# Performance work log

Measured on AMD Instinct MI355X. Metric: run time of the kernel, lower is better.

## Reference

```python
import jax, jax.numpy as jnp
import numpy as np

VOCAB, DIM, HEADS, LAYERS = 32000, 1024, 16, 2
B, S = 2, 1024
HD = DIM // HEADS


def rmsnorm(x, g, eps=1e-6):
    return x * jax.lax.rsqrt(jnp.mean(x * x, axis=-1, keepdims=True) + eps) * g


def setup_inputs() -> dict:
    key = jax.random.key(0)
    ks = jax.random.split(key, 20)
    s = 0.02
    d = {
        "text_ids": jax.random.randint(ks[0], (B, S), 0, VOCAB),
        "embed": jax.random.normal(ks[1], (VOCAB, DIM), jnp.float32) * s,
        "g1": jnp.ones((LAYERS, DIM), jnp.float32),
        "wq": jax.random.normal(ks[2], (LAYERS, DIM, DIM), jnp.float32) * s,
        "bq": jnp.zeros((LAYERS, DIM), jnp.float32),
        "wk": jax.random.normal(ks[3], (LAYERS, DIM, DIM), jnp.float32) * s,
        "bk": jnp.zeros((LAYERS, DIM), jnp.float32),
        "wv": jax.random.normal(ks[4], (LAYERS, DIM, DIM), jnp.float32) * s,
        "bv": jnp.zeros((LAYERS, DIM), jnp.float32),
        "wo": jax.random.normal(ks[5], (LAYERS, DIM, DIM), jnp.float32) * s,
        "bo": jnp.zeros((LAYERS, DIM), jnp.float32),
        "g2": jnp.ones((LAYERS, DIM), jnp.float32),
        "w1": jax.random.normal(ks[6], (LAYERS, DIM, 4 * DIM), jnp.float32) * s,
        "b1": jnp.zeros((LAYERS, 4 * DIM), jnp.float32),
        "w2": jax.random.normal(ks[7], (LAYERS, 4 * DIM, DIM), jnp.float32) * s,
        "b2": jnp.zeros((LAYERS, DIM), jnp.float32),
        "gf": jnp.ones((DIM,), jnp.float32),
        "head_w": jax.random.normal(ks[8], (DIM, VOCAB), jnp.float32) * s,
        "head_b": jnp.zeros((VOCAB,), jnp.float32),
    }
    return d


def reference(text_ids, embed, g1, wq, bq, wk, bk, wv, bv, wo, bo,
              g2, w1, b1, w2, b2, gf, head_w, head_b):
    b, s = text_ids.shape
    x = embed[text_ids]                                   # [B,S,D]
    causal = jnp.tril(jnp.ones((s, s), dtype=bool))        # [S,S]
    scale = 1.0 / jnp.sqrt(jnp.asarray(HD, x.dtype))
    for l in range(LAYERS):
        # attention sublayer: x = x + attn(norm1(x))
        h = rmsnorm(x, g1[l])
        q = (h @ wq[l] + bq[l]).reshape(b, s, HEADS, HD)
        k = (h @ wk[l] + bk[l]).reshape(b, s, HEADS, HD)
        v = (h @ wv[l] + bv[l]).reshape(b, s, HEADS, HD)
        scores = jnp.einsum("bqhd,bkhd->bhqk", q, k) * scale
        scores = jnp.where(causal, scores, jnp.asarray(-1e30, scores.dtype))
        a = jax.nn.softmax(scores, axis=-1)
        o = jnp.einsum("bhqk,bkhd->bqhd", a, v).reshape(b, s, DIM)
        x = x + (o @ wo[l] + bo[l])
        # FFN sublayer: x = x + ffn(norm2(x)), SiLU MLP (MoE unused in source forward)
        h2 = rmsnorm(x, g2[l])
        x = x + (jax.nn.silu(h2 @ w1[l] + b1[l]) @ w2[l] + b2[l])
    x = rmsnorm(x, gf)
    return x.astype(jnp.float32) @ head_w + head_b         # [B,S,VOCAB]
```

## Files before the change

### kernel.cpp

```cpp
#include <hip/hip_runtime.h>

#define LAYERS 2
#define DIM 1024
#define HEADS 16
#define HD 64
#define BATCH 2
#define SEQ 1024
#define ROWS (BATCH * SEQ)
#define FFN (4 * DIM)
#define VOCAB 32000
#define QKVN (3 * DIM)

typedef unsigned short u16;
typedef short vshort8 __attribute__((ext_vector_type(8)));
typedef float f32x4 __attribute__((ext_vector_type(4)));

#define VMCNT(n) asm volatile("s_waitcnt vmcnt(" #n ")" ::: "memory")

__device__ __forceinline__ u16 f2bf(float f) {
  union { float f; unsigned u; } x{f};
  unsigned r = (x.u + 0x7fffu + ((x.u >> 16) & 1u)) >> 16;
  return (u16)r;
}

__device__ __forceinline__ void gll16(const void* g, u16* l) {
  __builtin_amdgcn_global_load_lds(
      (const __attribute__((address_space(1))) void*)g,
      (__attribute__((address_space(3))) void*)l, 16, 0, 0);
}

__device__ __forceinline__ int xcd_swizzle(int orig, int nwg) {
  int q = nwg >> 3, r = nwg & 7;
  int xcd = orig & 7;
  int base = (xcd < r) ? xcd * (q + 1) : r * (q + 1) + (xcd - r) * q;
  return base + (orig >> 3);
}

__device__ __forceinline__ void trans64(const float* __restrict__ src,
                                        u16* __restrict__ dst, int C, int R,
                                        int r0, int c0, int tid,
                                        u16 (*tl)[72]) {
  int lr = tid >> 4, lc4 = (tid & 15) * 4;
#pragma unroll
  for (int i = 0; i < 4; i++) {
    int row = lr + i * 16;
    float4 v = *(const float4*)&src[(size_t)(r0 + row) * C + c0 + lc4];
    ushort4 o{f2bf(v.x), f2bf(v.y), f2bf(v.z), f2bf(v.w)};
    *(ushort4*)&tl[row][lc4] = o;
  }
  __syncthreads();
#pragma unroll
  for (int i = 0; i < 2; i++) {
    int idx = tid + i * 256;
    int ci = idx >> 3, ri0 = (idx & 7) * 8;
    vshort8 o;
#pragma unroll
    for (int j = 0; j < 8; j++) o[j] = (short)tl[ri0 + j][ci];
    *(vshort8*)&dst[(size_t)(c0 + ci) * R + r0 + ri0] = o;
  }
}

__global__ __launch_bounds__(256) void prologue_kernel(
    const float* __restrict__ wq, const float* __restrict__ wk,
    const float* __restrict__ wv, const float* __restrict__ wo,
    const float* __restrict__ w1, const float* __restrict__ w2,
    const float* __restrict__ head_w, const float* __restrict__ bq,
    const float* __restrict__ bk, const float* __restrict__ bv,
    const int* __restrict__ ids, const float* __restrict__ emb,
    const float* __restrict__ g1, u16* __restrict__ wqkvT,
    u16* __restrict__ woT, u16* __restrict__ w1T, u16* __restrict__ w2T,
    u16* __restrict__ headT, float* __restrict__ bqkv, float* __restrict__ x,
    u16* __restrict__ h) {
  __shared__ u16 tl[64][72];
  __shared__ float part[4];
  int bid = blockIdx.x, tid = threadIdx.x;
  if (bid >= 6144 && bid < 6168) {
    int t = (bid - 6144) * 256 + tid;
    int l = t / QKVN, c = t % QKVN;
    float v;
    if (c < DIM) v = bq[l * DIM + c];
    else if (c < 2 * DIM) v = bk[l * DIM + c - DIM];
    else v = bv[l * DIM + c - 2 * DIM];
    bqkv[(size_t)l * QKVN + c] = v;
    return;
  }
  if (bid >= 6168 && bid < 8216) {
    int row = bid - 6168;
    int id = ids[row];
    float4 v = ((const float4*)(emb + (size_t)id * DIM))[tid];
    ((float4*)(x + (size_t)row * DIM))[tid] = v;
    float ss = v.x * v.x + v.y * v.y + v.z * v.z + v.w * v.w;
    for (int off = 32; off > 0; off >>= 1) ss += __shfl_down(ss, off);
    if ((tid & 63) == 0) part[tid >> 6] = ss;
    __syncthreads();
    float tot = part[0] + part[1] + part[2] + part[3];
    float r = rsqrtf(tot / (float)DIM + 1e-6f);
    float4 gv = ((const float4*)g1)[tid];
    ushort4 o;
    o.x = f2bf(v.x * r * gv.x);
    o.y = f2bf(v.y * r * gv.y);
    o.z = f2bf(v.z * r * gv.z);
    o.w = f2bf(v.w * r * gv.w);
    *(ushort4*)(h + (size_t)row * DIM + tid * 4) = o;
    return;
  }
  const float* src;
  u16* dst;
  int R, C, r0, c0;
  if (bid < 2048) {
    int job = bid >> 8, tile = bid & 255;
    int l = job >> 2, wsel = job & 3;
    src = (wsel == 0 ? wq : wsel == 1 ? wk : wsel == 2 ? wv : wo) +
          (size_t)l * DIM * DIM;
    dst = (wsel < 3)
              ? wqkvT + (size_t)l * QKVN * DIM + (size_t)wsel * DIM * DIM
              : woT + (size_t)l * DIM * DIM;
    R = DIM; C = DIM;
    c0 = (tile & 15) * 64; r0 = (tile >> 4) * 64;
  } else if (bid < 4096) {
    int idx = bid - 2048;
    int l = idx >> 10, t = idx & 1023;
    src = w1 + (size_t)l * DIM * FFN;
    dst = w1T + (size_t)l * DIM * FFN;
    R = DIM; C = FFN;
    c0 = (t & 63) * 64; r0 = (t >> 6) * 64;
  } else if (bid < 6144) {
    int idx = bid - 4096;
    int l = idx >> 10, t = idx & 1023;
    src = w2 + (size_t)l * FFN * DIM;
    dst = w2T + (size_t)l * FFN * DIM;
    R = FFN; C = DIM;
    c0 = (t & 15) * 64; r0 = (t >> 4) * 64;
  } else {
    int t = bid - 8216;
    src = head_w; dst = headT;
    R = DIM; C = VOCAB;
    c0 = (t % 500) * 64; r0 = (t / 500) * 64;
  }
  trans64(src, dst, C, R, r0, c0, tid, tl);
}

template <int NP>
__global__ __launch_bounds__(256) void addnorm_kernel(
    float* __restrict__ x, const float* __restrict__ P,
    const float* __restrict__ bias, const float* __restrict__ g,
    u16* __restrict__ h) {
  int row = blockIdx.x;
  int t = threadIdx.x;
  float4 v = ((const float4*)(x + (size_t)row * DIM))[t];
  float4 c = ((const float4*)bias)[t];
  v.x += c.x; v.y += c.y; v.z += c.z; v.w += c.w;
#pragma unroll
  for (int p = 0; p < NP; p++) {
    float4 a = ((const float4*)(P + (size_t)p * ROWS * DIM + (size_t)row * DIM))[t];
    v.x += a.x; v.y += a.y; v.z += a.z; v.w += a.w;
  }
  ((float4*)(x + (size_t)row * DIM))[t] = v;
  float ss = v.x * v.x + v.y * v.y + v.z * v.z + v.w * v.w;
  for (int off = 32; off > 0; off >>= 1) ss += __shfl_down(ss, off);
  __shared__ float part[4];
  if ((t & 63) == 0) part[t >> 6] = ss;
  __syncthreads();
  float tot = part[0] + part[1] + part[2] + part[3];
  float r = rsqrtf(tot / (float)DIM + 1e-6f);
  float4 gv = ((const float4*)g)[t];
  ushort4 o;
  o.x = f2bf(v.x * r * gv.x);
  o.y = f2bf(v.y * r * gv.y);
  o.z = f2bf(v.z * r * gv.z);
  o.w = f2bf(v.w * r * gv.w);
  *(ushort4*)(h + (size_t)row * DIM + t * 4) = o;
}

template <int NMT, int OUTF32, int SILU, int VT>
__global__ __launch_bounds__(512, 2) void gemm256x128p_kernel(
    const u16* __restrict__ A, const u16* __restrict__ Wt,
    const float* __restrict__ bias, void* __restrict__ outv,
    u16* __restrict__ vt2, int M, int N, int K) {
  __shared__ u16 As[3][256 * 64];
  __shared__ u16 Bs[3][128 * 64];
  int nm = M >> 8, nn = N >> 7;
  int nwg = (NMT == 1) ? nm * nn : nn;
  int wg = xcd_swizzle(blockIdx.x, nwg);
  int mi0, ni;
  if (NMT == 1) { mi0 = wg % nm; ni = wg / nm; }
  else          { mi0 = 0; ni = wg; }
  int n0 = ni << 7;
  int tid = threadIdx.x, w = tid >> 6, lane = tid & 63;
  int wr = w >> 1, wc = w & 1;
  int r16 = lane & 15, g4 = lane >> 4;
  int srow8 = lane >> 3, sslot = lane & 7;
  const int NG = NMT * 16;

  f32x4 acc[4][4] = {};

  auto stage = [&](int g) {
    int buf = g % 3;
    int kt = g & 15;
    int mb = (mi0 + (g >> 4)) << 8;
#pragma unroll
    for (int j = 0; j < 4; j++) {
      int chunk = j * 8 + w;
      int row = chunk * 8 + srow8;
      int slot = sslot ^ (row & 7);
      gll16(A + (size_t)(mb + row) * K + kt * 64 + slot * 8,
            &As[buf][chunk * 512 + lane * 8]);
    }
#pragma unroll
    for (int j = 0; j < 2; j++) {
      int chunk = j * 8 + w;
      int row = chunk * 8 + srow8;
      int slot = sslot ^ (row & 7);
      gll16(Wt + (size_t)(n0 + row) * K + kt * 64 + slot * 8,
            &Bs[buf][chunk * 512 + lane * 8]);
    }
  };
  auto readA = [&](int buf, int mf, int kk) -> vshort8 {
    int row = wr * 64 + mf * 16 + r16;
    int slot = (kk * 4 + g4) ^ (row & 7);
    return *(const vshort8*)&As[buf][row * 64 + slot * 8];
  };
  auto readB = [&](int buf, int nf, int kk) -> vshort8 {
    int row = wc * 64 + nf * 16 + r16;
    int slot = (kk * 4 + g4) ^ (row & 7);
    return *(const vshort8*)&Bs[buf][row * 64 + slot * 8];
  };

  stage(0);
  stage(1);
  VMCNT(6);
  __builtin_amdgcn_s_barrier();

  vshort8 af[4][2], bf0[2][2], bf1[2][2];

  for (int mt = 0; mt < NMT; mt++) {
    for (int kt = 0; kt < 16; kt++) {
      int g = mt * 16 + kt;
      int buf = g % 3;
#pragma unroll
      for (int m = 0; m < 4; m++)
#pragma unroll
        for (int kk = 0; kk < 2; kk++) af[m][kk] = readA(buf, m, kk);
#pragma unroll
      for (int n = 0; n < 2; n++)
#pragma unroll
        for (int kk = 0; kk < 2; kk++) bf0[n][kk] = readB(buf, n, kk);
      bool staged = (g + 2 < NG);
      if (staged) stage(g + 2);
      __builtin_amdgcn_s_barrier();
      __builtin_amdgcn_s_setprio(1);
#pragma unroll
      for (int m = 0; m < 4; m++)
#pragma unroll
        for (int n = 0; n < 2; n++)
#pragma unroll
          for (int kk = 0; kk < 2; kk++)
            acc[m][n] = __builtin_amdgcn_mfma_f32_16x16x32_bf16(
                af[m][kk], bf0[n][kk], acc[m][n], 0, 0, 0);
      __builtin_amdgcn_s_setprio(0);
      __builtin_amdgcn_s_barrier();
#pragma unroll
      for (int n = 0; n < 2; n++)
#pragma unroll
        for (int kk = 0; kk < 2; kk++) bf1[n][kk] = readB(buf, 2 + n, kk);
      __builtin_amdgcn_s_barrier();
      __builtin_amdgcn_s_setprio(1);
#pragma unroll
      for (int m = 0; m < 4; m++)
#pragma unroll
        for (int n = 0; n < 2; n++)
#pragma unroll
          for (int kk = 0; kk < 2; kk++)
            acc[m][n + 2] = __builtin_amdgcn_mfma_f32_16x16x32_bf16(
                af[m][kk], bf1[n][kk], acc[m][n + 2], 0, 0, 0);
      __builtin_amdgcn_s_setprio(0);
      if (staged) { VMCNT(6); } else { VMCNT(0); }
      __builtin_amdgcn_s_barrier();
    }
    int m0e = (mi0 + mt) << 8;
#pragma unroll
    for (int m = 0; m < 4; m++) {
      int rowb = m0e + wr * 64 + m * 16 + g4 * 4;
#pragma unroll
      for (int n = 0; n < 4; n++) {
        int col = n0 + wc * 64 + n * 16 + r16;
        float b = bias[col];
        if (OUTF32) {
#pragma unroll
          for (int j = 0; j < 4; j++)
            ((float*)outv)[(size_t)(rowb + j) * N + col] = acc[m][n][j] + b;
        } else {
          u16 ov[4];
#pragma unroll
          for (int j = 0; j < 4; j++) {
            float v = acc[m][n][j] + b;
            if (SILU) v = v / (1.f + __expf(-v));
            ov[j] = f2bf(v);
          }
          if (VT && col >= 2 * DIM) {
            int dv = col - 2 * DIM;
            int hh = dv >> 6, dd = dv & 63;
            int bb = rowb >> 10, s = rowb & 1023;
            ushort4 o4{ov[0], ov[1], ov[2], ov[3]};
            *(ushort4*)&vt2[((((size_t)(bb * 16 + hh) * (SEQ / 8) + (s >> 3)) *
                                  64 + dd) * 8) + (s & 7)] = o4;
          } else {
#pragma unroll
            for (int j = 0; j < 4; j++)
              ((u16*)outv)[(size_t)(rowb + j) * N + col] = ov[j];
          }
        }
        if (NMT > 1) acc[m][n] = f32x4{0.f, 0.f, 0.f, 0.f};
      }
    }
  }
}

template <int NS>
__global__ __launch_bounds__(256, 2) void gemm128sk_kernel(
    const u16* __restrict__ A, const u16* __restrict__ Wt,
    float* __restrict__ P, int M, int N, int K) {
  __shared__ u16 As[2][128 * 64];
  __shared__ u16 Bs[2][128 * 64];
  int nm = M >> 7, nn = N >> 7, nwg = nm * nn;
  int wg = xcd_swizzle(blockIdx.x, nwg * NS);
  int ks = wg / nwg;
  wg -= ks * nwg;
  int ni = wg % nn, mi = wg / nn;
  int m0 = mi << 7, n0 = ni << 7;
  int kb = ks * (K / NS);
  int NTt = (K / NS) >> 6;
  int tid = threadIdx.x, wave = tid >> 6, lane = tid & 63;
  int wr = wave >> 1, wc = wave & 1;
  int r16 = lane & 15, g4 = lane >> 4;
  int lrow = lane >> 3, lslot = lane & 7;

  f32x4 acc[4][4] = {};

  auto stage = [&](int buf, int kt) {
#pragma unroll
    for (int i = 0; i < 4; i++) {
      int s = wave * 4 + i;
      int row = s * 8 + lrow;
      int slot = lslot ^ (row & 7);
      gll16(A + (size_t)(m0 + row) * K + kb + kt * 64 + slot * 8,
            &As[buf][s * 512 + lane * 8]);
    }
#pragma unroll
    for (int i = 0; i < 4; i++) {
      int s = wave * 4 + i;
      int row = s * 8 + lrow;
      int slot = lslot ^ (row & 7);
      gll16(Wt + (size_t)(n0 + row) * K + kb + kt * 64 + slot * 8,
            &Bs[buf][s * 512 + lane * 8]);
    }
  };

  stage(0, 0);
  VMCNT(0);
  __builtin_amdgcn_s_barrier();

  for (int t = 0; t < NTt; t++) {
    int cur = t & 1;
    if (t + 1 < NTt) stage(cur ^ 1, t + 1);
#pragma unroll
    for (int kk = 0; kk < 2; kk++) {
      vshort8 af[4], bf[4];
#pragma unroll
      for (int m = 0; m < 4; m++) {
        int r = wr * 64 + m * 16 + r16;
        int slot = (kk * 4 + g4) ^ (r & 7);
        af[m] = *(const vshort8*)&As[cur][r * 64 + slot * 8];
      }
#pragma unroll
      for (int n = 0; n < 4; n++) {
        int c = wc * 64 + n * 16 + r16;
        int slot = (kk * 4 + g4) ^ (c & 7);
        bf[n] = *(const vshort8*)&Bs[cur][c * 64 + slot * 8];
      }
#pragma unroll
      for (int m = 0; m < 4; m++)
#pragma unroll
        for (int n = 0; n < 4; n++)
          acc[m][n] = __builtin_amdgcn_mfma_f32_16x16x32_bf16(af[m], bf[n],
                                                              acc[m][n], 0, 0, 0);
    }
    VMCNT(0);
    __builtin_amdgcn_s_barrier();
  }

  float* Pk = P + (size_t)ks * M * N;
#pragma unroll
  for (int m = 0; m < 4; m++) {
    int rowb = m0 + wr * 64 + m * 16 + g4 * 4;
#pragma unroll
    for (int n = 0; n < 4; n++) {
      int col = n0 + wc * 64 + n * 16 + r16;
#pragma unroll
      for (int j = 0; j < 4; j++)
        Pk[(size_t)(rowb + j) * N + col] = acc[m][n][j];
    }
  }
}

__global__ __launch_bounds__(512, 2) void gemm256p_kernel(
    const u16* __restrict__ A, const u16* __restrict__ Wt,
    const float* __restrict__ bias, float* __restrict__ out,
    int M, int N, int K) {
  __shared__ u16 As[2][256 * 64];
  __shared__ u16 Bs[2][256 * 64];
  int nn = N >> 8;
  int wg = xcd_swizzle(blockIdx.x, nn * 2);
  int ni = wg >> 1, mhalf = wg & 1;
  int n0 = ni << 8;
  int tid = threadIdx.x, w = tid >> 6, lane = tid & 63;
  int wr = w >> 2, wc = w & 3;
  int r16 = lane & 15, g4 = lane >> 4;
  int srow8 = lane >> 3, sslot = lane & 7;
  const int NTK = 16;
  const int NGT = 64;

  f32x4 acc[8][4] = {};

  auto stageA = [&](int buf, int mb, int kt, int hb, int j) {
    int chunk = j * 8 + w;
    int row = hb * 128 + chunk * 8 + srow8;
    int slot = sslot ^ (row & 7);
    gll16(A + (size_t)(mb + row) * K + kt * 64 + slot * 8,
          &As[buf][hb * 8192 + chunk * 512 + lane * 8]);
  };
  auto stageB = [&](int buf, int kt, int hb, int j) {
    int chunk = j * 8 + w;
    int row = hb * 128 + chunk * 8 + srow8;
    int slot = sslot ^ (row & 7);
    gll16(Wt + (size_t)(n0 + row) * K + kt * 64 + slot * 8,
          &Bs[buf][hb * 8192 + chunk * 512 + lane * 8]);
  };
  auto readA = [&](int buf, int mf, int kk) -> vshort8 {
    int row = mf * 32 + wr * 16 + r16;
    int slot = (kk * 4 + g4) ^ (row & 7);
    return *(const vshort8*)&As[buf][row * 64 + slot * 8];
  };
  auto readB = [&](int buf, int nf, int kk) -> vshort8 {
    int row = nf * 64 + wc * 16 + r16;
    int slot = (kk * 4 + g4) ^ (row & 7);
    return *(const vshort8*)&Bs[buf][row * 64 + slot * 8];
  };

  int mb0 = (mhalf * 4) << 8;
  stageA(0, mb0, 0, 0, 0); stageA(0, mb0, 0, 0, 1);
  stageB(0, 0, 0, 0);      stageB(0, 0, 0, 1);
  stageB(0, 0, 1, 0);      stageB(0, 0, 1, 1);
  stageA(0, mb0, 0, 1, 0); stageA(0, mb0, 0, 1, 1);
  VMCNT(4);
  __builtin_amdgcn_s_barrier();

  vshort8 af[4][2], bf0[2][2], bf1[2][2];

  for (int ti = 0; ti < 4; ti++) {
    int m0 = (mhalf * 4 + ti) << 8;
    for (int tt = 0; tt < NTK; tt++) {
      int gt = ti * NTK + tt;
      int cur = gt & 1, nxt = cur ^ 1;
      int gt1 = gt + 1;
      bool hn = gt1 < NGT;
      int kt1 = gt1 & (NTK - 1);
      int mb1 = (mhalf * 4 + (gt1 >> 4)) << 8;
#pragma unroll
      for (int m = 0; m < 4; m++)
#pragma unroll
        for (int kk = 0; kk < 2; kk++) af[m][kk] = readA(cur, m, kk);
#pragma unroll
      for (int n = 0; n < 2; n++)
#pragma unroll
        for (int kk = 0; kk < 2; kk++) bf0[n][kk] = readB(cur, n, kk);
      if (hn) {
        stageA(nxt, mb1, kt1, 0, 0); stageA(nxt, mb1, kt1, 0, 1);
        stageB(nxt, kt1, 0, 0);      stageB(nxt, kt1, 0, 1);
      }
      __builtin_amdgcn_s_barrier();
      __builtin_amdgcn_s_setprio(1);
#pragma unroll
      for (int m = 0; m < 4; m++)
#pragma unroll
        for (int n = 0; n < 2; n++)
#pragma unroll
          for (int kk = 0; kk < 2; kk++)
            acc[m][n] = __builtin_amdgcn_mfma_f32_16x16x32_bf16(
                af[m][kk], bf0[n][kk], acc[m][n], 0, 0, 0);
      __builtin_amdgcn_s_setprio(0);
      VMCNT(4);
      __builtin_amdgcn_s_barrier();
#pragma unroll
      for (int n = 0; n < 2; n++)
#pragma unroll
        for (int kk = 0; kk < 2; kk++) bf1[n][kk] = readB(cur, 2 + n, kk);
      __builtin_amdgcn_s_barrier();
      __builtin_amdgcn_s_setprio(1);
#pragma unroll
      for (int m = 0; m < 4; m++)
#pragma unroll
        for (int n = 0; n < 2; n++)
#pragma unroll
          for (int kk = 0; kk < 2; kk++)
            acc[m][n + 2] = __builtin_amdgcn_mfma_f32_16x16x32_bf16(
                af[m][kk], bf1[n][kk], acc[m][n + 2], 0, 0, 0);
      __builtin_amdgcn_s_setprio(0);
      __builtin_amdgcn_s_barrier();
#pragma unroll
      for (int m = 0; m < 4; m++)
#pragma unroll
        for (int kk = 0; kk < 2; kk++) af[m][kk] = readA(cur, 4 + m, kk);
      if (hn) {
        stageB(nxt, kt1, 1, 0);      stageB(nxt, kt1, 1, 1);
        stageA(nxt, mb1, kt1, 1, 0); stageA(nxt, mb1, kt1, 1, 1);
      }
      __builtin_amdgcn_s_barrier();
      __builtin_amdgcn_s_setprio(1);
#pragma unroll
      for (int m = 0; m < 4; m++)
#pragma unroll
        for (int n = 0; n < 2; n++)
#pragma unroll
          for (int kk = 0; kk < 2; kk++)
            acc[m + 4][n + 2] = __builtin_amdgcn_mfma_f32_16x16x32_bf16(
                af[m][kk], bf1[n][kk], acc[m + 4][n + 2], 0, 0, 0);
#pragma unroll
      for (int m = 0; m < 4; m++)
#pragma unroll
        for (int n = 0; n < 2; n++)
#pragma unroll
          for (int kk = 0; kk < 2; kk++)
            acc[m + 4][n] = __builtin_amdgcn_mfma_f32_16x16x32_bf16(
                af[m][kk], bf0[n][kk], acc[m + 4][n], 0, 0, 0);
      __builtin_amdgcn_s_setprio(0);
      VMCNT(4);
      __builtin_amdgcn_s_barrier();
    }
#pragma unroll
    for (int mf = 0; mf < 8; mf++) {
      int rowb = m0 + mf * 32 + wr * 16 + g4 * 4;
#pragma unroll
      for (int nf = 0; nf < 4; nf++) {
        int col = n0 + nf * 64 + wc * 16 + r16;
        float b = bias[col];
#pragma unroll
        for (int j = 0; j < 4; j++)
          out[(size_t)(rowb + j) * N + col] = acc[mf][nf][j] + b;
      }
    }
#pragma unroll
    for (int mf = 0; mf < 8; mf++)
#pragma unroll
      for (int nf = 0; nf < 4; nf++) acc[mf][nf] = f32x4{0.f, 0.f, 0.f, 0.f};
  }
}

__global__ __launch_bounds__(256) void attn_kernel(const u16* __restrict__ qkv,
                                                   const u16* __restrict__ vt2,
                                                   u16* __restrict__ o) {
  __shared__ u16 Ks[2][32 * 64];
  __shared__ u16 pl[4][16 * 40];
  int qblk = blockIdx.x, bh = blockIdx.y;
  int b = bh >> 4, h = bh & 15;
  int tid = threadIdx.x, w = tid >> 6, lane = tid & 63;
  int r16 = lane & 15, g4 = lane >> 4;
  int q0 = qblk * 64 + w * 16;

  const u16* qrow = qkv + ((size_t)(b * SEQ) + q0 + r16) * QKVN + h * HD;
  vshort8 aq0 = *(const vshort8*)(qrow + g4 * 8);
  vshort8 aq1 = *(const vshort8*)(qrow + 32 + g4 * 8);

  float mrun[4], lrun[4];
  f32x4 accO[4];
#pragma unroll
  for (int j = 0; j < 4; j++) { mrun[j] = -1e30f; lrun[j] = 0.f; }
#pragma unroll
  for (int d = 0; d < 4; d++) accO[d] = f32x4{0.f, 0.f, 0.f, 0.f};

  int nkvT = qblk * 2 + 2;
  auto stageK = [&](int buf, int kt) {
    int row = tid >> 3;
    int slot = (tid & 7) ^ (row & 7);
    gll16(qkv + ((size_t)(b * SEQ) + kt * 32 + row) * QKVN + DIM + h * HD + slot * 8,
          &Ks[buf][w * 512 + lane * 8]);
  };
  stageK(0, 0);
  __syncthreads();
  int buf = 0;
  for (int kt = 0; kt < nkvT; kt++) {
    int kv0 = kt * 32;
    if (kt + 1 < nkvT) stageK(buf ^ 1, kt + 1);
    if (kv0 <= q0 + 15) {
      int row0 = r16, row1 = 16 + r16;
      vshort8 bk00 = *(const vshort8*)&Ks[buf][row0 * 64 + ((0 + g4) ^ (row0 & 7)) * 8];
      vshort8 bk01 = *(const vshort8*)&Ks[buf][row0 * 64 + ((4 + g4) ^ (row0 & 7)) * 8];
      vshort8 bk10 = *(const vshort8*)&Ks[buf][row1 * 64 + ((0 + g4) ^ (row1 & 7)) * 8];
      vshort8 bk11 = *(const vshort8*)&Ks[buf][row1 * 64 + ((4 + g4) ^ (row1 & 7)) * 8];
      f32x4 s0 = {}, s1 = {};
      s0 = __builtin_amdgcn_mfma_f32_16x16x32_bf16(aq0, bk00, s0, 0, 0, 0);
      s0 = __builtin_amdgcn_mfma_f32_16x16x32_bf16(aq1, bk01, s0, 0, 0, 0);
      s1 = __builtin_amdgcn_mfma_f32_16x16x32_bf16(aq0, bk10, s1, 0, 0, 0);
      s1 = __builtin_amdgcn_mfma_f32_16x16x32_bf16(aq1, bk11, s1, 0, 0, 0);

#pragma unroll
      for (int j = 0; j < 4; j++) {
        int qg = q0 + g4 * 4 + j;
        float x0 = s0[j] * 0.125f;
        float x1 = s1[j] * 0.125f;
        if (kv0 + r16 > qg) x0 = -1e30f;
        if (kv0 + 16 + r16 > qg) x1 = -1e30f;
        float mx = fmaxf(x0, x1);
#pragma unroll
        for (int mm = 1; mm < 16; mm <<= 1) mx = fmaxf(mx, __shfl_xor(mx, mm));
        float mnew = fmaxf(mrun[j], mx);
        float alpha = __expf(mrun[j] - mnew);
        float p0 = __expf(x0 - mnew);
        float p1 = __expf(x1 - mnew);
        float rs = p0 + p1;
#pragma unroll
        for (int mm = 1; mm < 16; mm <<= 1) rs += __shfl_xor(rs, mm);
        lrun[j] = lrun[j] * alpha + rs;
        mrun[j] = mnew;
#pragma unroll
        for (int d = 0; d < 4; d++) accO[d][j] *= alpha;
        pl[w][(g4 * 4 + j) * 40 + r16] = f2bf(p0);
        pl[w][(g4 * 4 + j) * 40 + 16 + r16] = f2bf(p1);
      }
      asm volatile("s_waitcnt lgkmcnt(0)" ::: "memory");
      vshort8 ap = *(const vshort8*)&pl[w][r16 * 40 + g4 * 8];
      const u16* vbase = vt2 + (((size_t)bh * (SEQ / 8) + (kv0 >> 3) + g4) * 64) * 8;
#pragma unroll
      for (int d = 0; d < 4; d++) {
        vshort8 bv = *(const vshort8*)(vbase + (size_t)(d * 16 + r16) * 8);
        accO[d] = __builtin_amdgcn_mfma_f32_16x16x32_bf16(ap, bv, accO[d], 0, 0, 0);
      }
    }
    __syncthreads();
    buf ^= 1;
  }

#pragma unroll
  for (int j = 0; j < 4; j++) {
    float inv = 1.f / lrun[j];
    int row = q0 + g4 * 4 + j;
#pragma unroll
    for (int d = 0; d < 4; d++)
      o[((size_t)(b * SEQ) + row) * DIM + h * HD + d * 16 + r16] =
          f2bf(accO[d][j] * inv);
  }
}

extern "C" void kernel_launch(void* const* d_in, const int* in_sizes, int n_in,
                              void* d_out, int out_size, void* d_ws,
                              size_t ws_size, hipStream_t stream) {
  const int* ids = (const int*)d_in[0];
  const float* emb = (const float*)d_in[1];
  const float* g1 = (const float*)d_in[2];
  const float* wq = (const float*)d_in[3];
  const float* bq = (const float*)d_in[4];
  const float* wk = (const float*)d_in[5];
  const float* bk = (const float*)d_in[6];
  const float* wv = (const float*)d_in[7];
  const float* bv = (const float*)d_in[8];
  const float* wo = (const float*)d_in[9];
  const float* bo = (const float*)d_in[10];
  const float* g2 = (const float*)d_in[11];
  const float* w1 = (const float*)d_in[12];
  const float* b1 = (const float*)d_in[13];
  const float* w2 = (const float*)d_in[14];
  const float* b2 = (const float*)d_in[15];
  const float* gf = (const float*)d_in[16];
  const float* head_w = (const float*)d_in[17];
  const float* head_b = (const float*)d_in[18];
  float* out = (float*)d_out;

  char* ws = (char*)d_ws;
  size_t off = 0;
  auto alloc = [&](size_t bytes) -> char* {
    char* p = ws + off;
    off += (bytes + 255) & ~(size_t)255;
    return p;
  };
  u16* wqkvT = (u16*)alloc((size_t)LAYERS * QKVN * DIM * 2);
  u16* woT = (u16*)alloc((size_t)LAYERS * DIM * DIM * 2);
  u16* w1T = (u16*)alloc((size_t)LAYERS * DIM * FFN * 2);
  u16* w2T = (u16*)alloc((size_t)LAYERS * DIM * FFN * 2);
  u16* headT = (u16*)alloc((size_t)VOCAB * DIM * 2);
  float* bqkv = (float*)alloc((size_t)LAYERS * QKVN * 4);
  float* x = (float*)alloc((size_t)ROWS * DIM * 4);
  u16* h = (u16*)alloc((size_t)ROWS * DIM * 2);
  u16* qkvb = (u16*)alloc((size_t)ROWS * QKVN * 2);
  u16* vtb = (u16*)alloc((size_t)ROWS * DIM * 2);
  u16* ob = (u16*)alloc((size_t)ROWS * DIM * 2);
  u16* tb = (u16*)alloc((size_t)ROWS * FFN * 2);
  float* P = (float*)alloc((size_t)4 * ROWS * DIM * 4);
  if (off > ws_size) return;

  prologue_kernel<<<16216, 256, 0, stream>>>(
      wq, wk, wv, wo, w1, w2, head_w, bq, bk, bv, ids, emb, g1, wqkvT, woT,
      w1T, w2T, headT, bqkv, x, h);

  for (int l = 0; l < LAYERS; l++) {
    gemm256x128p_kernel<1, 0, 0, 1>
        <<<(ROWS / 256) * (QKVN / 128), 512, 0, stream>>>(
            h, wqkvT + (size_t)l * QKVN * DIM, bqkv + (size_t)l * QKVN,
            qkvb, vtb, ROWS, QKVN, DIM);
    attn_kernel<<<dim3(SEQ / 64, BATCH * HEADS), 256, 0, stream>>>(qkvb, vtb, ob);
    gemm128sk_kernel<4>
        <<<4 * (ROWS / 128) * (DIM / 128), 256, 0, stream>>>(
            ob, woT + (size_t)l * DIM * DIM, P, ROWS, DIM, DIM);
    addnorm_kernel<4><<<ROWS, 256, 0, stream>>>(
        x, P, bo + (size_t)l * DIM, g2 + (size_t)l * DIM, h);
    gemm256x128p_kernel<1, 0, 1, 0>
        <<<(ROWS / 256) * (FFN / 128), 512, 0, stream>>>(
            h, w1T + (size_t)l * DIM * FFN, b1 + (size_t)l * FFN, tb, nullptr,
            ROWS, FFN, DIM);
    gemm128sk_kernel<4>
        <<<4 * (ROWS / 128) * (DIM / 128), 256, 0, stream>>>(
            tb, w2T + (size_t)l * DIM * FFN, P, ROWS, DIM, FFN);
    addnorm_kernel<4><<<ROWS, 256, 0, stream>>>(
        x, P, b2 + (size_t)l * DIM,
        (l == LAYERS - 1) ? gf : (g1 + (size_t)(l + 1) * DIM), h);
  }
  gemm256p_kernel<<<(VOCAB / 256) * 2, 512, 0, stream>>>(
      h, headT, head_b, out, ROWS, VOCAB, DIM);
}
```

Baseline: 558.6 us.

## Rewrite LM-head GEMM with triple-buffered K=32 stages and a single MFMA phase

Replaces the double-buffered K=64 LM-head GEMM, which split each step into several MFMA phases with interleaved loads and barriers, with a triple-buffered pipeline over K=32 tiles that prefetches two stages ahead. Each iteration now does one block of LDS reads, one issue of global-to-LDS loads and one MFMA burst, with a single barrier per step, and uses a new XOR swizzle for the narrower tiles. Launch bounds drop from two blocks per CU to one. The intent is to hide memory latency with fewer barriers, at the cost of occupancy and of twice as many k-steps, each carrying a barrier.

```diff
diff --git a/kernel.cpp b/kernel.cpp
--- a/kernel.cpp
+++ b/kernel.cpp
@@ -403,12 +403,12 @@
   }
 }
 
-__global__ __launch_bounds__(512, 2) void gemm256p_kernel(
+__global__ __launch_bounds__(512, 1) void gemm256h_kernel(
     const u16* __restrict__ A, const u16* __restrict__ Wt,
     const float* __restrict__ bias, float* __restrict__ out,
     int M, int N, int K) {
-  __shared__ u16 As[2][256 * 64];
-  __shared__ u16 Bs[2][256 * 64];
+  __shared__ u16 As[3][256 * 32];
+  __shared__ u16 Bs[3][256 * 32];
   int nn = N >> 8;
   int wg = xcd_swizzle(blockIdx.x, nn * 2);
   int ni = wg >> 1, mhalf = wg & 1;
@@ -416,143 +416,81 @@
   int tid = threadIdx.x, w = tid >> 6, lane = tid & 63;
   int wr = w >> 2, wc = w & 3;
   int r16 = lane & 15, g4 = lane >> 4;
-  int srow8 = lane >> 3, sslot = lane & 7;
-  const int NTK = 16;
-  const int NGT = 64;
+  const int NG = 128;
 
   f32x4 acc[8][4] = {};
 
-  auto stageA = [&](int buf, int mb, int kt, int hb, int j) {
-    int chunk = j * 8 + w;
-    int row = hb * 128 + chunk * 8 + srow8;
-    int slot = sslot ^ (row & 7);
-    gll16(A + (size_t)(mb + row) * K + kt * 64 + slot * 8,
-          &As[buf][hb * 8192 + chunk * 512 + lane * 8]);
+  int srow = w * 16 + (lane >> 2);
+  int schunk = lane & 3;
+
+  auto stage = [&](int g) {
+    int buf = g % 3;
+    int kt = g & 31;
+    int mb = (mhalf * 4 + (g >> 5)) << 8;
+#pragma unroll
+    for (int u = 0; u < 2; u++) {
+      int row = u * 128 + srow;
+      int klog = (schunk ^ ((row >> 1) & 3)) * 8;
+      gll16(A + (size_t)(mb + row) * K + kt * 32 + klog,
+            &As[buf][u * 4096 + w * 512 + lane * 8]);
+    }
+#pragma unroll
+    for (int u = 0; u < 2; u++) {
+      int row = u * 128 + srow;
+      int klog = (schunk ^ ((row >> 1) & 3)) * 8;
+      gll16(Wt + (size_t)(n0 + row) * K + kt * 32 + klog,
+            &Bs[buf][u * 4096 + w * 512 + lane * 8]);
+    }
   };
-  auto stageB = [&](int buf, int kt, int hb, int j) {
-    int chunk = j * 8 + w;
-    int row = hb * 128 + chunk * 8 + srow8;
-    int slot = sslot ^ (row & 7);
-    gll16(Wt + (size_t)(n0 + row) * K + kt * 64 + slot * 8,
-          &Bs[buf][hb * 8192 + chunk * 512 + lane * 8]);
-  };
-  auto readA = [&](int buf, int mf, int kk) -> vshort8 {
-    int row = mf * 32 + wr * 16 + r16;
-    int slot = (kk * 4 + g4) ^ (row & 7);
-    return *(const vshort8*)&As[buf][row * 64 + slot * 8];
-  };
-  auto readB = [&](int buf, int nf, int kk) -> vshort8 {
-    int row = nf * 64 + wc * 16 + r16;
-    int slot = (kk * 4 + g4) ^ (row & 7);
-    return *(const vshort8*)&Bs[buf][row * 64 + slot * 8];
-  };
-
-  int mb0 = (mhalf * 4) << 8;
-  stageA(0, mb0, 0, 0, 0); stageA(0, mb0, 0, 0, 1);
-  stageB(0, 0, 0, 0);      stageB(0, 0, 0, 1);
-  stageB(0, 0, 1, 0);      stageB(0, 0, 1, 1);
-  stageA(0, mb0, 0, 1, 0); stageA(0, mb0, 0, 1, 1);
+
+  stage(0);
+  stage(1);
   VMCNT(4);
   __builtin_amdgcn_s_barrier();
 
-  vshort8 af[4][2], bf0[2][2], bf1[2][2];
-
-  for (int ti = 0; ti < 4; ti++) {
-    int m0 = (mhalf * 4 + ti) << 8;
-    for (int tt = 0; tt < NTK; tt++) {
-      int gt = ti * NTK + tt;
-      int cur = gt & 1, nxt = cur ^ 1;
-      int gt1 = gt + 1;
-      bool hn = gt1 < NGT;
-      int kt1 = gt1 & (NTK - 1);
-      int mb1 = (mhalf * 4 + (gt1 >> 4)) << 8;
-#pragma unroll
-      for (int m = 0; m < 4; m++)
-#pragma unroll
-        for (int kk = 0; kk < 2; kk++) af[m][kk] = readA(cur, m, kk);
-#pragma unroll
-      for (int n = 0; n < 2; n++)
-#pragma unroll
-        for (int kk = 0; kk < 2; kk++) bf0[n][kk] = readB(cur, n, kk);
-      if (hn) {
-        stageA(nxt, mb1, kt1, 0, 0); stageA(nxt, mb1, kt1, 0, 1);
-        stageB(nxt, kt1, 0, 0);      stageB(nxt, kt1, 0, 1);
+  for (int g = 0; g < NG; g++) {
+    int buf = g % 3;
+    vshort8 af[8], bf[4];
+#pragma unroll
+    for (int m = 0; m < 8; m++) {
+      int row = m * 32 + wr * 16 + r16;
+      int s = g4 ^ ((row >> 1) & 3);
+      af[m] = *(const vshort8*)&As[buf][row * 32 + s * 8];
+    }
+#pragma unroll
+    for (int n = 0; n < 4; n++) {
+      int row = n * 64 + wc * 16 + r16;
+      int s = g4 ^ ((row >> 1) & 3);
+      bf[n] = *(const vshort8*)&Bs[buf][row * 32 + s * 8];
+    }
+    bool staged = (g + 2 < NG);
+    if (staged) stage(g + 2);
+    __builtin_amdgcn_s_setprio(1);
+#pragma unroll
+    for (int m = 0; m < 8; m++)
+#pragma unroll
+      for (int n = 0; n < 4; n++)
+        acc[m][n] = __builtin_amdgcn_mfma_f32_16x16x32_bf16(af[m], bf[n],
+                                                            acc[m][n], 0, 0, 0);
+    __builtin_amdgcn_s_setprio(0);
+    if (staged) { VMCNT(4); } else { VMCNT(0); }
+    __builtin_amdgcn_s_barrier();
+    if ((g & 31) == 31) {
+      int m0 = (mhalf * 4 + (g >> 5)) << 8;
+#pragma unroll
+      for (int mf = 0; mf < 8; mf++) {
+        int rowb = m0 + mf * 32 + wr * 16 + g4 * 4;
+#pragma unroll
+        for (int nf = 0; nf < 4; nf++) {
+          int col = n0 + nf * 64 + wc * 16 + r16;
+          float b = bias[col];
+#pragma unroll
+          for (int j = 0; j < 4; j++)
+            out[(size_t)(rowb + j) * N + col] = acc[mf][nf][j] + b;
+          acc[mf][nf] = f32x4{0.f, 0.f, 0.f, 0.f};
+        }
       }
-      __builtin_amdgcn_s_barrier();
-      __builtin_amdgcn_s_setprio(1);
-#pragma unroll
-      for (int m = 0; m < 4; m++)
-#pragma unroll
-        for (int n = 0; n < 2; n++)
-#pragma unroll
-          for (int kk = 0; kk < 2; kk++)
-            acc[m][n] = __builtin_amdgcn_mfma_f32_16x16x32_bf16(
-                af[m][kk], bf0[n][kk], acc[m][n], 0, 0, 0);
-      __builtin_amdgcn_s_setprio(0);
-      VMCNT(4);
-      __builtin_amdgcn_s_barrier();
-#pragma unroll
-      for (int n = 0; n < 2; n++)
-#pragma unroll
-        for (int kk = 0; kk < 2; kk++) bf1[n][kk] = readB(cur, 2 + n, kk);
-      __builtin_amdgcn_s_barrier();
-      __builtin_amdgcn_s_setprio(1);
-#pragma unroll
-      for (int m = 0; m < 4; m++)
-#pragma unroll
-        for (int n = 0; n < 2; n++)
-#pragma unroll
-          for (int kk = 0; kk < 2; kk++)
-            acc[m][n + 2] = __builtin_amdgcn_mfma_f32_16x16x32_bf16(
-                af[m][kk], bf1[n][kk], acc[m][n + 2], 0, 0, 0);
-      __builtin_amdgcn_s_setprio(0);
-      __builtin_amdgcn_s_barrier();
-#pragma unroll
-      for (int m = 0; m < 4; m++)
-#pragma unroll
-        for (int kk = 0; kk < 2; kk++) af[m][kk] = readA(cur, 4 + m, kk);
-      if (hn) {
-        stageB(nxt, kt1, 1, 0);      stageB(nxt, kt1, 1, 1);
-        stageA(nxt, mb1, kt1, 1, 0); stageA(nxt, mb1, kt1, 1, 1);
-      }
-      __builtin_amdgcn_s_barrier();
-      __builtin_amdgcn_s_setprio(1);
-#pragma unroll
-      for (int m = 0; m < 4; m++)
-#pragma unroll
-        for (int n = 0; n < 2; n++)
-#pragma unroll
-          for (int kk = 0; kk < 2; kk++)
-            acc[m + 4][n + 2] = __builtin_amdgcn_mfma_f32_16x16x32_bf16(
-                af[m][kk], bf1[n][kk], acc[m + 4][n + 2], 0, 0, 0);
-#pragma unroll
-      for (int m = 0; m < 4; m++)
-#pragma unroll
-        for (int n = 0; n < 2; n++)
-#pragma unroll
-          for (int kk = 0; kk < 2; kk++)
-            acc[m + 4][n] = __builtin_amdgcn_mfma_f32_16x16x32_bf16(
-                af[m][kk], bf0[n][kk], acc[m + 4][n], 0, 0, 0);
-      __builtin_amdgcn_s_setprio(0);
-      VMCNT(4);
-      __builtin_amdgcn_s_barrier();
-    }
-#pragma unroll
-    for (int mf = 0; mf < 8; mf++) {
-      int rowb = m0 + mf * 32 + wr * 16 + g4 * 4;
-#pragma unroll
-      for (int nf = 0; nf < 4; nf++) {
-        int col = n0 + nf * 64 + wc * 16 + r16;
-        float b = bias[col];
-#pragma unroll
-        for (int j = 0; j < 4; j++)
-          out[(size_t)(rowb + j) * N + col] = acc[mf][nf][j] + b;
-      }
-    }
-#pragma unroll
-    for (int mf = 0; mf < 8; mf++)
-#pragma unroll
-      for (int nf = 0; nf < 4; nf++) acc[mf][nf] = f32x4{0.f, 0.f, 0.f, 0.f};
+    }
   }
 }
 
@@ -723,6 +661,6 @@
         x, P, b2 + (size_t)l * DIM,
         (l == LAYERS - 1) ? gf : (g1 + (size_t)(l + 1) * DIM), h);
   }
-  gemm256p_kernel<<<(VOCAB / 256) * 2, 512, 0, stream>>>(
+  gemm256h_kernel<<<(VOCAB / 256) * 2, 512, 0, stream>>>(
       h, headT, head_b, out, ROWS, VOCAB, DIM);
 }
```

New measurement: 563.9 us. No clear change (+1.0%).
